# Kernel optimization log

Measured on AMD Instinct MI355X. Metric: run time of the kernel, lower is better.

Reference implementation:

```python
import jax, jax.numpy as jnp
import numpy as np

D_MODEL = 2048
N_HEADS = 16
N_KV_HEADS = 4
HEAD_DIM = D_MODEL // N_HEADS  # 128
WINDOW = 512
THETA = 10000.0


def rotate_half(x):
    x1, x2 = jnp.split(x, 2, axis=-1)
    return jnp.concatenate((-x2, x1), axis=-1)


def rope_cos_sin(seq_len, dtype=jnp.float32):
    inv_freq = 1.0 / (THETA ** (jnp.arange(0, HEAD_DIM, 2, dtype=jnp.float32) / HEAD_DIM))
    t = jnp.arange(seq_len, dtype=jnp.float32)
    freqs = jnp.outer(t, inv_freq)              # [S, HEAD_DIM/2]
    emb = jnp.concatenate((freqs, freqs), -1)   # [S, HEAD_DIM]
    return jnp.cos(emb).astype(dtype), jnp.sin(emb).astype(dtype)


def setup_inputs() -> dict:
    key = jax.random.key(0)
    ks = jax.random.split(key, 5)
    B, S = 2, 2048
    sc = 1.0 / np.sqrt(D_MODEL)
    return {
        "x": jax.random.normal(ks[0], (B, S, D_MODEL), jnp.float32),
        "wq": jax.random.normal(ks[1], (D_MODEL, N_HEADS * HEAD_DIM), jnp.float32) * sc,
        "wk": jax.random.normal(ks[2], (D_MODEL, N_KV_HEADS * HEAD_DIM), jnp.float32) * sc,
        "wv": jax.random.normal(ks[3], (D_MODEL, N_KV_HEADS * HEAD_DIM), jnp.float32) * sc,
        "wo": jax.random.normal(ks[4], (N_HEADS * HEAD_DIM, D_MODEL), jnp.float32) * sc,
    }


def reference(x, wq, wk, wv, wo):
    B, S, _ = x.shape
    n_rep = N_HEADS // N_KV_HEADS

    q = (x @ wq).reshape(B, S, N_HEADS, HEAD_DIM).transpose(0, 2, 1, 3)      # [B,H,S,D]
    k = (x @ wk).reshape(B, S, N_KV_HEADS, HEAD_DIM).transpose(0, 2, 1, 3)   # [B,KVH,S,D]
    v = (x @ wv).reshape(B, S, N_KV_HEADS, HEAD_DIM).transpose(0, 2, 1, 3)

    cos, sin = rope_cos_sin(S, x.dtype)  # [S, D]
    q = q * cos + rotate_half(q) * sin
    k = k * cos + rotate_half(k) * sin

    # GQA: repeat kv heads to match query heads
    k = jnp.repeat(k, n_rep, axis=1)  # [B,H,S,D]
    v = jnp.repeat(v, n_rep, axis=1)

    scale = 1.0 / np.sqrt(HEAD_DIM)
    scores = jnp.einsum("bhqd,bhkd->bhqk", q, k) * scale

    # causal + sliding-window mask: allow i-WINDOW+1 <= j <= i
    i = jnp.arange(S)[:, None]
    j = jnp.arange(S)[None, :]
    allowed = (j <= i) & (j >= i - WINDOW + 1)
    scores = jnp.where(allowed, scores, -jnp.inf)

    attn = jax.nn.softmax(scores.astype(jnp.float32), axis=-1).astype(x.dtype)
    out = jnp.einsum("bhqk,bhkd->bhqd", attn, v)          # [B,H,S,D]
    out = out.transpose(0, 2, 1, 3).reshape(B, S, N_HEADS * HEAD_DIM)
    return out @ wo
```

## Files before the change

kernel.cpp:

```cpp
#include <hip/hip_runtime.h>
#include <math.h>


typedef unsigned short u16;
typedef __attribute__((ext_vector_type(4))) float f32x4;
typedef __attribute__((ext_vector_type(8))) __bf16 bf16x8;
typedef __attribute__((ext_vector_type(4))) __bf16 bf16x4;
typedef __attribute__((ext_vector_type(4))) short s16x4;
typedef __attribute__((ext_vector_type(8))) unsigned short u16x8;
typedef __attribute__((ext_vector_type(4))) unsigned short u16x4;

#define DEV static __device__ __forceinline__

DEV float bf2f(u16 h) {
    union { unsigned int i; float f; } x;
    x.i = ((unsigned int)h) << 16;
    return x.f;
}
DEV u16 f2bf(float f) {
    union { float f; unsigned int i; } x;
    x.f = f;
    unsigned int u = x.i;
    return (u16)((u + 0x7FFFu + ((u >> 16) & 1u)) >> 16);
}

DEV f32x4 mfma32(bf16x8 a, bf16x8 b, f32x4 c) {
    return __builtin_amdgcn_mfma_f32_16x16x32_bf16(a, b, c, 0, 0, 0);
}
DEV f32x4 mfma16(bf16x4 a, bf16x4 b, f32x4 c) {
#if __has_builtin(__builtin_amdgcn_mfma_f32_16x16x16_bf16)
    return __builtin_amdgcn_mfma_f32_16x16x16_bf16(a, b, c, 0, 0, 0);
#else
    union { bf16x4 v; s16x4 s; } ua, ub;
    ua.v = a; ub.v = b;
    return __builtin_amdgcn_mfma_f32_16x16x16bf16_1k(ua.s, ub.s, c, 0, 0, 0);
#endif
}

DEV void gload_lds16(const void* g, void* lds) {
    __builtin_amdgcn_global_load_lds(
        (const __attribute__((address_space(1))) unsigned int*)g,
        (__attribute__((address_space(3))) unsigned int*)lds, 16, 0, 0);
}

__global__ __launch_bounds__(256) void prep_kernel(const float* x, const float* wq,
                                                   const float* wk, const float* wv,
                                                   const float* wo, u16* xb, u16* wAll,
                                                   u16* woT, float* ct, float* st) {
    __shared__ float tile[32][33];
    const int bid = blockIdx.x;
    const int tid = threadIdx.x;
    if (bid < 512) {
        int idx = bid * 256 + tid;
        int s = idx >> 6, d = idx & 63;
        float inv = exp2f(-(float)d * (13.287712379549449f / 64.f));
        float a = (float)s * inv;
        float sv, cv;
        sincosf(a, &sv, &cv);
        ct[idx] = cv;
        st[idx] = sv;
        return;
    }
    if (bid < 8704) {
        int i = (bid - 512) * 256 + tid;
        float4 v = ((const float4*)x)[i];
        u16x4 o;
        o[0] = f2bf(v.x); o[1] = f2bf(v.y); o[2] = f2bf(v.z); o[3] = f2bf(v.w);
        ((u16x4*)xb)[i] = o;
        return;
    }
    int r = bid - 8704;
    const float* in;
    u16* out;
    int ldi, bx, by;
    if (r < 4096) { in = wq; out = wAll; ldi = 2048; bx = r & 63; by = r >> 6; }
    else if (r < 5120) { r -= 4096; in = wk; out = wAll + (long)2048 * 2048; ldi = 512; bx = r & 15; by = r >> 4; }
    else if (r < 6144) { r -= 5120; in = wv; out = wAll + (long)2560 * 2048; ldi = 512; bx = r & 15; by = r >> 4; }
    else { r -= 6144; in = wo; out = woT; ldi = 2048; bx = r & 63; by = r >> 6; }
    int cc = tid & 31, rb = tid >> 5;
    long r0 = (long)by * 32, c0 = (long)bx * 32;
#pragma unroll
    for (int i = 0; i < 4; i++)
        tile[rb + i * 8][cc] = in[(r0 + rb + i * 8) * (long)ldi + c0 + cc];
    __syncthreads();
#pragma unroll
    for (int i = 0; i < 4; i++)
        out[(c0 + rb + i * 8) * 2048L + r0 + cc] = f2bf(tile[cc][rb + i * 8]);
}

__global__ __launch_bounds__(256) void transpose_bf16_kernel(const u16* in, int ldi, long in_bs,
                                                             u16* out, int ldo, long out_bs) {
    __shared__ u16 tile[32][33];
    in += (long)blockIdx.z * in_bs;
    out += (long)blockIdx.z * out_bs;
    int cc = threadIdx.x & 31, rb = threadIdx.x >> 5;
    long r0 = (long)blockIdx.y * 32, c0 = (long)blockIdx.x * 32;
#pragma unroll
    for (int i = 0; i < 4; i++)
        tile[rb + i * 8][cc] = in[(r0 + rb + i * 8) * (long)ldi + c0 + cc];
    __syncthreads();
#pragma unroll
    for (int i = 0; i < 4; i++)
        out[(c0 + rb + i * 8) * (long)ldo + r0 + cc] = tile[cc][rb + i * 8];
}

__global__ __launch_bounds__(256) void rope2_kernel(u16* QKV, const float* ct, const float* st) {
    int idx = blockIdx.x * 256 + threadIdx.x;
    int m, hoff, d0;
    if (idx < 524288) {
        m = idx >> 7;
        int rest = idx & 127;
        hoff = (rest >> 3) * 128;
        d0 = (rest & 7) * 8;
    } else {
        int i2 = idx - 524288;
        m = i2 >> 5;
        int rest = i2 & 31;
        hoff = 2048 + (rest >> 3) * 128;
        d0 = (rest & 7) * 8;
    }
    int s = m & 2047;
    u16* p1 = QKV + (long)m * 3072 + hoff + d0;
    u16* p2 = p1 + 64;
    u16x8 v1 = *(const u16x8*)p1;
    u16x8 v2 = *(const u16x8*)p2;
    const float* cp = ct + s * 64 + d0;
    const float* sp = st + s * 64 + d0;
    u16x8 o1, o2;
#pragma unroll
    for (int j = 0; j < 8; j++) {
        float x1 = bf2f(v1[j]), x2 = bf2f(v2[j]);
        float cc = cp[j], ss = sp[j];
        o1[j] = f2bf(x1 * cc - x2 * ss);
        o2[j] = f2bf(x2 * cc + x1 * ss);
    }
    *(u16x8*)p1 = o1;
    *(u16x8*)p2 = o2;
}

template <bool OUT_BF16>
__global__ __launch_bounds__(256) void gemm_bt_kernel(const u16* A, const u16* Bt, void* Cout,
                                                      int M, int N, int K) {
    __shared__ u16 As[2][128 * 32];
    __shared__ u16 Bs[2][128 * 32];
    const int tid = threadIdx.x;
    const int w = tid >> 6, l = tid & 63, g = l >> 4, c = l & 15;
    const int wm = w >> 1, wn = w & 1;
    const long m0 = (long)blockIdx.y * 128, n0 = (long)blockIdx.x * 128;
    const int nk = K >> 5;

    f32x4 acc[4][4];
    const f32x4 zero = {0.f, 0.f, 0.f, 0.f};
#pragma unroll
    for (int i = 0; i < 4; i++)
#pragma unroll
        for (int j = 0; j < 4; j++) acc[i][j] = zero;

    auto stage = [&](int buf, int kt) {
#pragma unroll
        for (int i = 0; i < 2; i++) {
            int o = (i * 256 + tid) * 16;
            int row = o >> 6;
            int cl = ((o >> 4) & 3) ^ ((row >> 1) & 3);
            gload_lds16(A + (m0 + row) * (long)K + kt * 32 + cl * 8,
                        (void*)&As[buf][(i * 256 + w * 64) * 8]);
        }
#pragma unroll
        for (int i = 0; i < 2; i++) {
            int o = (i * 256 + tid) * 16;
            int row = o >> 6;
            int cl = ((o >> 4) & 3) ^ ((row >> 1) & 3);
            gload_lds16(Bt + (n0 + row) * (long)K + kt * 32 + cl * 8,
                        (void*)&Bs[buf][(i * 256 + w * 64) * 8]);
        }
    };

    stage(0, 0);
    __syncthreads();
    int buf = 0;
    for (int kt = 0; kt < nk; ++kt) {
        if (kt + 1 < nk) stage(buf ^ 1, kt + 1);
        bf16x8 af[4], bf[4];
#pragma unroll
        for (int i = 0; i < 4; i++) {
            int rowa = wm * 64 + i * 16 + c;
            int cha = g ^ ((rowa >> 1) & 3);
            af[i] = *(const bf16x8*)&As[buf][rowa * 32 + cha * 8];
            int rowb = wn * 64 + i * 16 + c;
            int chb = g ^ ((rowb >> 1) & 3);
            bf[i] = *(const bf16x8*)&Bs[buf][rowb * 32 + chb * 8];
        }
#pragma unroll
        for (int i = 0; i < 4; i++)
#pragma unroll
            for (int j = 0; j < 4; j++) acc[i][j] = mfma32(af[i], bf[j], acc[i][j]);
        __syncthreads();
        buf ^= 1;
    }

#pragma unroll
    for (int i = 0; i < 4; i++)
#pragma unroll
        for (int j = 0; j < 4; j++) {
            long row0 = m0 + wm * 64 + i * 16 + g * 4;
            long col = n0 + wn * 64 + j * 16 + c;
#pragma unroll
            for (int r = 0; r < 4; r++) {
                float v = acc[i][j][r];
                if (OUT_BF16)
                    ((u16*)Cout)[(row0 + r) * (long)N + col] = f2bf(v);
                else
                    ((float*)Cout)[(row0 + r) * (long)N + col] = v;
            }
        }
}

#define ATT_SCALE 0.08838834764831845f
#define L2E 1.4426950408889634f

__global__ __launch_bounds__(512) void attn_kernel(const u16* QKV, const u16* Vt, u16* AO) {
    __shared__ u16 Ks[2][64 * 128];
    __shared__ u16 Vs[2][128 * 64];
    const int tid = threadIdx.x;
    const int w = tid >> 6, l = tid & 63, g = l >> 4, c = l & 15;
    const int h = blockIdx.y;
    const int b = blockIdx.z;
    const int kvh = h >> 2;
    const int q0 = blockIdx.x * 128;
    const int qb = q0 + w * 16;

    bf16x8 bq[4];
    {
        const u16* qrow = QKV + (long)(b * 2048 + qb + c) * 3072 + h * 128;
#pragma unroll
        for (int kc = 0; kc < 4; kc++) bq[kc] = *(const bf16x8*)(qrow + kc * 32 + g * 8);
    }

    f32x4 acc_o[8];
    const f32x4 zero = {0.f, 0.f, 0.f, 0.f};
#pragma unroll
    for (int i = 0; i < 8; i++) acc_o[i] = zero;
    float m_run = -3.0e38f, l_run = 0.f;

    const int t_lo = (q0 > 511) ? ((q0 - 511) >> 6) : 0;
    const int t_hi = (q0 + 127) >> 6;

    auto stage = [&](int sb, int t) {
        const int kv0 = t * 64;
#pragma unroll
        for (int i = 0; i < 2; i++) {
            int o = (i * 512 + tid) * 16;
            int key = o >> 8;
            int cl = ((o >> 4) & 15) ^ (key & 15);
            gload_lds16(QKV + (long)(b * 2048 + kv0 + key) * 3072 + 2048 + kvh * 128 + cl * 8,
                        (void*)&Ks[sb][(i * 512 + w * 64) * 8]);
        }
#pragma unroll
        for (int i = 0; i < 2; i++) {
            int o = (i * 512 + tid) * 16;
            int d = o >> 7;
            int cl = ((o >> 4) & 7) ^ (d & 7);
            gload_lds16(Vt + (long)((b * 4 + kvh) * 128 + d) * 2048 + kv0 + cl * 8,
                        (void*)&Vs[sb][(i * 512 + w * 64) * 8]);
        }
    };

    stage(0, t_lo);
    __syncthreads();
    int buf = 0;

    for (int t = t_lo; t <= t_hi; ++t) {
        const int kv0 = t * 64;
        if (t < t_hi) stage(buf ^ 1, t + 1);

        const bool active = (kv0 <= qb + 15) && (kv0 + 63 >= qb - 511);
        if (active) {
            f32x4 sacc[4];
#pragma unroll
            for (int n = 0; n < 4; n++) {
                sacc[n] = zero;
#pragma unroll
                for (int kc = 0; kc < 4; kc++) {
                    int row = n * 16 + c;
                    int ch = (kc * 4 + g) ^ c;
                    bf16x8 kf = *(const bf16x8*)&Ks[buf][row * 128 + ch * 8];
                    sacc[n] = mfma32(kf, bq[kc], sacc[n]);
                }
            }

            const bool edge = (kv0 + 63 > qb) || (kv0 < qb + 15 - 511);
            float p[4][4];
            float m_tile = -3.0e38f;
#pragma unroll
            for (int n = 0; n < 4; n++)
#pragma unroll
                for (int r = 0; r < 4; r++) {
                    float s = sacc[n][r] * ATT_SCALE;
                    if (edge) {
                        int j = kv0 + n * 16 + 4 * g + r;
                        int q = qb + c;
                        if (j > q || j < q - 511) s = -__builtin_inff();
                    }
                    p[n][r] = s;
                    m_tile = fmaxf(m_tile, s);
                }
            m_tile = fmaxf(m_tile, __shfl_xor(m_tile, 16));
            m_tile = fmaxf(m_tile, __shfl_xor(m_tile, 32));
            float m_new = fmaxf(m_run, m_tile);
            float alpha = exp2f((m_run - m_new) * L2E);
            float lsum = 0.f;
#pragma unroll
            for (int n = 0; n < 4; n++)
#pragma unroll
                for (int r = 0; r < 4; r++) {
                    float e = exp2f((p[n][r] - m_new) * L2E);
                    p[n][r] = e;
                    lsum += e;
                }
            lsum += __shfl_xor(lsum, 16);
            lsum += __shfl_xor(lsum, 32);
            l_run = l_run * alpha + lsum;
            m_run = m_new;

            float alpha_r[4];
#pragma unroll
            for (int r = 0; r < 4; r++) alpha_r[r] = __shfl(alpha, (g << 4) + 4 * g + r);
#pragma unroll
            for (int dn = 0; dn < 8; dn++) {
                f32x4 t2 = acc_o[dn];
                t2[0] *= alpha_r[0]; t2[1] *= alpha_r[1];
                t2[2] *= alpha_r[2]; t2[3] *= alpha_r[3];
                acc_o[dn] = t2;
            }

            bf16x4 ap[4];
#pragma unroll
            for (int n = 0; n < 4; n++) {
                union { u16x4 u; bf16x4 b; } pk;
                pk.u[0] = f2bf(p[n][0]); pk.u[1] = f2bf(p[n][1]);
                pk.u[2] = f2bf(p[n][2]); pk.u[3] = f2bf(p[n][3]);
                ap[n] = pk.b;
            }

#pragma unroll
            for (int n = 0; n < 4; n++)
#pragma unroll
                for (int dn = 0; dn < 8; dn++) {
                    int row = dn * 16 + c;
                    int ch = (2 * n + (g >> 1)) ^ (c & 7);
                    bf16x4 vf = *(const bf16x4*)&Vs[buf][row * 64 + ch * 8 + (g & 1) * 4];
                    acc_o[dn] = mfma16(ap[n], vf, acc_o[dn]);
                }
        }
        __syncthreads();
        buf ^= 1;
    }

    float lr[4];
#pragma unroll
    for (int r = 0; r < 4; r++) {
        float lq = __shfl(l_run, (g << 4) + 4 * g + r);
        lr[r] = 1.f / lq;
    }
#pragma unroll
    for (int dn = 0; dn < 8; dn++)
#pragma unroll
        for (int r = 0; r < 4; r++) {
            long row = (long)(b * 2048 + qb + 4 * g + r);
            AO[row * 2048 + h * 128 + dn * 16 + c] = f2bf(acc_o[dn][r] * lr[r]);
        }
}

extern "C" void kernel_launch(void* const* d_in, const int* in_sizes, int n_in,
                              void* d_out, int out_size, void* d_ws, size_t ws_size,
                              hipStream_t stream) {
    const float* x = (const float*)d_in[0];
    const float* wq = (const float*)d_in[1];
    const float* wk = (const float*)d_in[2];
    const float* wv = (const float*)d_in[3];
    const float* wo = (const float*)d_in[4];
    float* out = (float*)d_out;

    char* ws = (char*)d_ws;
    u16* xb = (u16*)(ws);
    u16* wAll = (u16*)(ws + 16777216);
    u16* woT = (u16*)(ws + 29360128);
    u16* QKV = (u16*)(ws + 37748736);
    u16* Vt = (u16*)(ws + 62914560);
    u16* AO = (u16*)(ws + 67108864);
    float* ct = (float*)(ws + 83886080);
    float* st = (float*)(ws + 84410368);

    prep_kernel<<<18944, 256, 0, stream>>>(x, wq, wk, wv, wo, xb, wAll, woT, ct, st);

    gemm_bt_kernel<true><<<dim3(24, 32), 256, 0, stream>>>(xb, wAll, QKV, 4096, 3072, 2048);

    rope2_kernel<<<2560, 256, 0, stream>>>(QKV, ct, st);

    transpose_bf16_kernel<<<dim3(16, 64, 2), 256, 0, stream>>>(
        QKV + 2560, 3072, (long)2048 * 3072, Vt, 2048, (long)512 * 2048);

    attn_kernel<<<dim3(16, 16, 2), 512, 0, stream>>>(QKV, Vt, AO);

    gemm_bt_kernel<false><<<dim3(16, 32), 256, 0, stream>>>(AO, woT, out, 4096, 2048, 2048);
}
```

Before: 182.1 us.

## Fuse Q RoPE into attention, merge K RoPE with V transpose, lazy rescale

Q rotary embedding now runs inside the attention kernel on the register-held Q fragments. The K-only RoPE and the V transpose are merged into one launch, which removes a kernel launch and a full read/write pass over Q. The online softmax also skips the rescaling of the accumulator and the running sum whenever no lane's tile max exceeds the running max by more than a threshold. Skipping rescale lets exp values grow up to 2^(8*log2e) before renormalization, which risks precision drift in bf16 P but avoids the per-tile multiply and shuffle work.

```diff
diff --git a/kernel.cpp b/kernel.cpp
--- a/kernel.cpp
+++ b/kernel.cpp
@@ -88,54 +88,51 @@
         out[(c0 + rb + i * 8) * 2048L + r0 + cc] = f2bf(tile[cc][rb + i * 8]);
 }
 
-__global__ __launch_bounds__(256) void transpose_bf16_kernel(const u16* in, int ldi, long in_bs,
-                                                             u16* out, int ldo, long out_bs) {
+__global__ __launch_bounds__(256) void ropeKT_kernel(u16* QKV, u16* Vt,
+                                                     const float* ct, const float* st) {
     __shared__ u16 tile[32][33];
-    in += (long)blockIdx.z * in_bs;
-    out += (long)blockIdx.z * out_bs;
-    int cc = threadIdx.x & 31, rb = threadIdx.x >> 5;
-    long r0 = (long)blockIdx.y * 32, c0 = (long)blockIdx.x * 32;
-#pragma unroll
-    for (int i = 0; i < 4; i++)
-        tile[rb + i * 8][cc] = in[(r0 + rb + i * 8) * (long)ldi + c0 + cc];
+    const int bid = blockIdx.x;
+    const int tid = threadIdx.x;
+    if (bid < 512) {
+        int idx = bid * 256 + tid;
+        int m = idx >> 5;
+        int rest = idx & 31;
+        int hoff = 2048 + (rest >> 3) * 128;
+        int d0 = (rest & 7) * 8;
+        int s = m & 2047;
+        u16* p1 = QKV + (long)m * 3072 + hoff + d0;
+        u16* p2 = p1 + 64;
+        u16x8 v1 = *(const u16x8*)p1;
+        u16x8 v2 = *(const u16x8*)p2;
+        const float* cp = ct + s * 64 + d0;
+        const float* sp = st + s * 64 + d0;
+        u16x8 o1, o2;
+#pragma unroll
+        for (int j = 0; j < 8; j++) {
+            float x1 = bf2f(v1[j]), x2 = bf2f(v2[j]);
+            float cc = cp[j], ss = sp[j];
+            o1[j] = f2bf(x1 * cc - x2 * ss);
+            o2[j] = f2bf(x2 * cc + x1 * ss);
+        }
+        *(u16x8*)p1 = o1;
+        *(u16x8*)p2 = o2;
+        return;
+    }
+    int r = bid - 512;
+    int z = r >> 10;
+    int rr = r & 1023;
+    int bx = rr & 15, by = rr >> 4;
+    const u16* in = QKV + 2560 + (long)z * 2048 * 3072;
+    u16* out = Vt + (long)z * 512 * 2048;
+    int cc = tid & 31, rb = tid >> 5;
+    long r0 = (long)by * 32, c0 = (long)bx * 32;
+#pragma unroll
+    for (int i = 0; i < 4; i++)
+        tile[rb + i * 8][cc] = in[(r0 + rb + i * 8) * 3072 + c0 + cc];
     __syncthreads();
 #pragma unroll
     for (int i = 0; i < 4; i++)
-        out[(c0 + rb + i * 8) * (long)ldo + r0 + cc] = tile[cc][rb + i * 8];
-}
-
-__global__ __launch_bounds__(256) void rope2_kernel(u16* QKV, const float* ct, const float* st) {
-    int idx = blockIdx.x * 256 + threadIdx.x;
-    int m, hoff, d0;
-    if (idx < 524288) {
-        m = idx >> 7;
-        int rest = idx & 127;
-        hoff = (rest >> 3) * 128;
-        d0 = (rest & 7) * 8;
-    } else {
-        int i2 = idx - 524288;
-        m = i2 >> 5;
-        int rest = i2 & 31;
-        hoff = 2048 + (rest >> 3) * 128;
-        d0 = (rest & 7) * 8;
-    }
-    int s = m & 2047;
-    u16* p1 = QKV + (long)m * 3072 + hoff + d0;
-    u16* p2 = p1 + 64;
-    u16x8 v1 = *(const u16x8*)p1;
-    u16x8 v2 = *(const u16x8*)p2;
-    const float* cp = ct + s * 64 + d0;
-    const float* sp = st + s * 64 + d0;
-    u16x8 o1, o2;
-#pragma unroll
-    for (int j = 0; j < 8; j++) {
-        float x1 = bf2f(v1[j]), x2 = bf2f(v2[j]);
-        float cc = cp[j], ss = sp[j];
-        o1[j] = f2bf(x1 * cc - x2 * ss);
-        o2[j] = f2bf(x2 * cc + x1 * ss);
-    }
-    *(u16x8*)p1 = o1;
-    *(u16x8*)p2 = o2;
+        out[(c0 + rb + i * 8) * 2048L + r0 + cc] = tile[cc][rb + i * 8];
 }
 
 template <bool OUT_BF16>
@@ -218,7 +215,8 @@
 #define ATT_SCALE 0.08838834764831845f
 #define L2E 1.4426950408889634f
 
-__global__ __launch_bounds__(512) void attn_kernel(const u16* QKV, const u16* Vt, u16* AO) {
+__global__ __launch_bounds__(512) void attn_kernel(const u16* QKV, const u16* Vt, u16* AO,
+                                                   const float* ct, const float* st) {
     __shared__ u16 Ks[2][64 * 128];
     __shared__ u16 Vs[2][128 * 64];
     const int tid = threadIdx.x;
@@ -234,6 +232,21 @@
         const u16* qrow = QKV + (long)(b * 2048 + qb + c) * 3072 + h * 128;
 #pragma unroll
         for (int kc = 0; kc < 4; kc++) bq[kc] = *(const bf16x8*)(qrow + kc * 32 + g * 8);
+        const float* cb = ct + (qb + c) * 64 + g * 8;
+        const float* sb = st + (qb + c) * 64 + g * 8;
+#pragma unroll
+        for (int kc = 0; kc < 2; kc++) {
+            union { bf16x8 v; u16x8 u; } lo, hi;
+            lo.v = bq[kc]; hi.v = bq[kc + 2];
+#pragma unroll
+            for (int j = 0; j < 8; j++) {
+                float x1 = bf2f(lo.u[j]), x2 = bf2f(hi.u[j]);
+                float cc = cb[kc * 32 + j], ss = sb[kc * 32 + j];
+                lo.u[j] = f2bf(x1 * cc - x2 * ss);
+                hi.u[j] = f2bf(x2 * cc + x1 * ss);
+            }
+            bq[kc] = lo.v; bq[kc + 2] = hi.v;
+        }
     }
 
     f32x4 acc_o[8];
@@ -245,7 +258,7 @@
     const int t_lo = (q0 > 511) ? ((q0 - 511) >> 6) : 0;
     const int t_hi = (q0 + 127) >> 6;
 
-    auto stage = [&](int sb, int t) {
+    auto stage = [&](int sb_, int t) {
         const int kv0 = t * 64;
 #pragma unroll
         for (int i = 0; i < 2; i++) {
@@ -253,7 +266,7 @@
             int key = o >> 8;
             int cl = ((o >> 4) & 15) ^ (key & 15);
             gload_lds16(QKV + (long)(b * 2048 + kv0 + key) * 3072 + 2048 + kvh * 128 + cl * 8,
-                        (void*)&Ks[sb][(i * 512 + w * 64) * 8]);
+                        (void*)&Ks[sb_][(i * 512 + w * 64) * 8]);
         }
 #pragma unroll
         for (int i = 0; i < 2; i++) {
@@ -261,7 +274,7 @@
             int d = o >> 7;
             int cl = ((o >> 4) & 7) ^ (d & 7);
             gload_lds16(Vt + (long)((b * 4 + kvh) * 128 + d) * 2048 + kv0 + cl * 8,
-                        (void*)&Vs[sb][(i * 512 + w * 64) * 8]);
+                        (void*)&Vs[sb_][(i * 512 + w * 64) * 8]);
         }
     };
 
@@ -306,8 +319,10 @@
                 }
             m_tile = fmaxf(m_tile, __shfl_xor(m_tile, 16));
             m_tile = fmaxf(m_tile, __shfl_xor(m_tile, 32));
-            float m_new = fmaxf(m_run, m_tile);
-            float alpha = exp2f((m_run - m_new) * L2E);
+
+            const bool keep = __all(m_tile - m_run <= 8.f);
+            const float m_new = keep ? m_run : fmaxf(m_run, m_tile);
+
             float lsum = 0.f;
 #pragma unroll
             for (int n = 0; n < 4; n++)
@@ -319,18 +334,23 @@
                 }
             lsum += __shfl_xor(lsum, 16);
             lsum += __shfl_xor(lsum, 32);
-            l_run = l_run * alpha + lsum;
-            m_run = m_new;
-
-            float alpha_r[4];
-#pragma unroll
-            for (int r = 0; r < 4; r++) alpha_r[r] = __shfl(alpha, (g << 4) + 4 * g + r);
-#pragma unroll
-            for (int dn = 0; dn < 8; dn++) {
-                f32x4 t2 = acc_o[dn];
-                t2[0] *= alpha_r[0]; t2[1] *= alpha_r[1];
-                t2[2] *= alpha_r[2]; t2[3] *= alpha_r[3];
-                acc_o[dn] = t2;
+
+            if (!keep) {
+                float alpha = exp2f((m_run - m_new) * L2E);
+                l_run = l_run * alpha + lsum;
+                m_run = m_new;
+                float alpha_r[4];
+#pragma unroll
+                for (int r = 0; r < 4; r++) alpha_r[r] = __shfl(alpha, (g << 4) + 4 * g + r);
+#pragma unroll
+                for (int dn = 0; dn < 8; dn++) {
+                    f32x4 t2 = acc_o[dn];
+                    t2[0] *= alpha_r[0]; t2[1] *= alpha_r[1];
+                    t2[2] *= alpha_r[2]; t2[3] *= alpha_r[3];
+                    acc_o[dn] = t2;
+                }
+            } else {
+                l_run += lsum;
             }
 
             bf16x4 ap[4];
@@ -395,12 +415,9 @@
 
     gemm_bt_kernel<true><<<dim3(24, 32), 256, 0, stream>>>(xb, wAll, QKV, 4096, 3072, 2048);
 
-    rope2_kernel<<<2560, 256, 0, stream>>>(QKV, ct, st);
-
-    transpose_bf16_kernel<<<dim3(16, 64, 2), 256, 0, stream>>>(
-        QKV + 2560, 3072, (long)2048 * 3072, Vt, 2048, (long)512 * 2048);
-
-    attn_kernel<<<dim3(16, 16, 2), 512, 0, stream>>>(QKV, Vt, AO);
+    ropeKT_kernel<<<2560, 256, 0, stream>>>(QKV, Vt, ct, st);
+
+    attn_kernel<<<dim3(16, 16, 2), 512, 0, stream>>>(QKV, Vt, AO, ct, st);
 
     gemm_bt_kernel<false><<<dim3(16, 32), 256, 0, stream>>>(AO, woT, out, 4096, 2048, 2048);
 }
```

New measurement: 178.1 us. -2.2%, faster.
